# Optimization experiments

Hardware: AMD Instinct MI355X
Metric: run time of the kernel (lower is better)

The kernel has to match this reference:

```python
import jax, jax.numpy as jnp
import numpy as np

HIDDEN = 1024
EMB = 256
VOCAB = 500000
B = 4096
C = 128
EPS = 1e-12


def setup_inputs() -> dict:
    key = jax.random.key(0)
    ks = jax.random.split(key, 8)
    hidden_states = jax.random.normal(ks[0], (B, HIDDEN), dtype=jnp.float32)
    cand_idx = jax.random.randint(ks[1], (B, C), 0, VOCAB, dtype=jnp.int32)
    W_dense = jax.random.normal(ks[2], (EMB, HIDDEN), dtype=jnp.float32) * (1.0 / np.sqrt(HIDDEN))
    b_dense = jnp.zeros((EMB,), dtype=jnp.float32)
    ln_gamma = jnp.ones((EMB,), dtype=jnp.float32)
    ln_beta = jnp.zeros((EMB,), dtype=jnp.float32)
    decoder_table = jax.random.normal(ks[3], (VOCAB, EMB), dtype=jnp.float32) * 0.02
    entity_bias = jnp.zeros((VOCAB,), dtype=jnp.float32)
    return {
        "hidden_states": hidden_states,
        "W_dense": W_dense,
        "b_dense": b_dense,
        "ln_gamma": ln_gamma,
        "ln_beta": ln_beta,
        "decoder_table": decoder_table,
        "entity_bias": entity_bias,
        "cand_idx": cand_idx,
    }


def _transform(x, W_dense, b_dense, ln_gamma, ln_beta):
    # Linear hidden_size -> entity_emb_size, gelu, LayerNorm
    h = x @ W_dense.T + b_dense
    h = jax.nn.gelu(h, approximate=False)
    mu = jnp.mean(h, axis=-1, keepdims=True)
    var = jnp.mean(jnp.square(h - mu), axis=-1, keepdims=True)
    return (h - mu) * jax.lax.rsqrt(var + EPS) * ln_gamma + ln_beta


def reference(hidden_states, W_dense, b_dense, ln_gamma, ln_beta, decoder_table, entity_bias, cand_idx):
    h = _transform(hidden_states, W_dense, b_dense, ln_gamma, ln_beta)  # [B, EMB]
    cand_emb = decoder_table[cand_idx]          # [B, C, EMB] ragged gather (padded)
    bias = entity_bias[cand_idx]                # [B, C]
    scores = jnp.einsum('bce,be->bc', cand_emb, h) + bias  # [B, C]
    return scores
```

## Files before the change

### kernel.cpp

```cpp
#include <hip/hip_runtime.h>
#include <hip/hip_bf16.h>
#include <math.h>

#define HIDDEN 1024
#define EMB    256
#define BROWS  4096
#define CAND   128
#define LN_EPS 1e-12f

typedef __attribute__((ext_vector_type(8))) short bf16x8;
typedef __attribute__((ext_vector_type(4))) float f32x4;

__device__ __forceinline__ int swz(int row, int slot) { return slot ^ ((row >> 1) & 3); }

__device__ __forceinline__ unsigned short f2bf(float f) {
    __bf16 h = (__bf16)f;
    return __builtin_bit_cast(unsigned short, h);
}

__global__ __launch_bounds__(256) void k_transform(
    const float* __restrict__ A,
    const float* __restrict__ W,
    const float* __restrict__ bias,
    const float* __restrict__ gamma,
    const float* __restrict__ beta,
    float* __restrict__ G)
{
    __shared__ unsigned short As[64 * 32];
    __shared__ unsigned short Ws[256 * 32];
    __shared__ float part[64][8];

    const int tid  = threadIdx.x;
    const int lane = tid & 63;
    const int wv   = tid >> 6;
    const int m0   = blockIdx.x * 64;

    const int lcol = lane & 15;
    const int lk   = lane >> 4;

    const int arow = tid >> 2;
    const int apr  = tid & 3;

    f32x4 acc[4][4] = {};

    for (int kt = 0; kt < HIDDEN; kt += 32) {
        float4 a0 = *(const float4*)&A[(size_t)(m0 + arow) * HIDDEN + kt + apr * 8];
        float4 a1 = *(const float4*)&A[(size_t)(m0 + arow) * HIDDEN + kt + apr * 8 + 4];
        float4 w0[4], w1[4];
        #pragma unroll
        for (int i = 0; i < 4; ++i) {
            int id = tid + i * 256;
            int row = id >> 2, pr = id & 3;
            w0[i] = *(const float4*)&W[(size_t)row * HIDDEN + kt + pr * 8];
            w1[i] = *(const float4*)&W[(size_t)row * HIDDEN + kt + pr * 8 + 4];
        }
        __syncthreads();
        {
            bf16x8 v;
            v[0]=f2bf(a0.x); v[1]=f2bf(a0.y); v[2]=f2bf(a0.z); v[3]=f2bf(a0.w);
            v[4]=f2bf(a1.x); v[5]=f2bf(a1.y); v[6]=f2bf(a1.z); v[7]=f2bf(a1.w);
            *(bf16x8*)&As[arow * 32 + swz(arow, apr) * 8] = v;
        }
        #pragma unroll
        for (int i = 0; i < 4; ++i) {
            int id = tid + i * 256;
            int row = id >> 2, pr = id & 3;
            bf16x8 v;
            v[0]=f2bf(w0[i].x); v[1]=f2bf(w0[i].y); v[2]=f2bf(w0[i].z); v[3]=f2bf(w0[i].w);
            v[4]=f2bf(w1[i].x); v[5]=f2bf(w1[i].y); v[6]=f2bf(w1[i].z); v[7]=f2bf(w1[i].w);
            *(bf16x8*)&Ws[row * 32 + swz(row, pr) * 8] = v;
        }
        __syncthreads();
        bf16x8 af[4], bfr[4];
        #pragma unroll
        for (int m = 0; m < 4; ++m) {
            int r = m * 16 + lcol;
            af[m] = *(const bf16x8*)&As[r * 32 + swz(r, lk) * 8];
        }
        #pragma unroll
        for (int n = 0; n < 4; ++n) {
            int r = wv * 64 + n * 16 + lcol;
            bfr[n] = *(const bf16x8*)&Ws[r * 32 + swz(r, lk) * 8];
        }
        #pragma unroll
        for (int m = 0; m < 4; ++m)
            #pragma unroll
            for (int n = 0; n < 4; ++n)
                acc[m][n] = __builtin_amdgcn_mfma_f32_16x16x32_bf16(af[m], bfr[n], acc[m][n], 0, 0, 0);
    }

    float bcol[4], gcol[4], becol[4];
    #pragma unroll
    for (int n = 0; n < 4; ++n) {
        int col = wv * 64 + n * 16 + lcol;
        bcol[n]  = bias[col];
        gcol[n]  = gamma[col];
        becol[n] = beta[col];
    }

    float sv[4][4], qv[4][4];
    #pragma unroll
    for (int m = 0; m < 4; ++m) {
        #pragma unroll
        for (int r = 0; r < 4; ++r) { sv[m][r] = 0.0f; qv[m][r] = 0.0f; }
        #pragma unroll
        for (int n = 0; n < 4; ++n) {
            #pragma unroll
            for (int r = 0; r < 4; ++r) {
                float v = acc[m][n][r] + bcol[n];
                v = 0.5f * v * (1.0f + erff(v * 0.70710678118654752f));
                acc[m][n][r] = v;
                sv[m][r] += v;
                qv[m][r] += v * v;
            }
        }
        #pragma unroll
        for (int r = 0; r < 4; ++r) {
            #pragma unroll
            for (int msk = 8; msk >= 1; msk >>= 1) {
                sv[m][r] += __shfl_xor(sv[m][r], msk);
                qv[m][r] += __shfl_xor(qv[m][r], msk);
            }
        }
    }
    if (lcol == 0) {
        #pragma unroll
        for (int m = 0; m < 4; ++m)
            #pragma unroll
            for (int r = 0; r < 4; ++r) {
                int R = m * 16 + lk * 4 + r;
                part[R][wv * 2 + 0] = sv[m][r];
                part[R][wv * 2 + 1] = qv[m][r];
            }
    }
    __syncthreads();

    #pragma unroll
    for (int m = 0; m < 4; ++m) {
        #pragma unroll
        for (int r = 0; r < 4; ++r) {
            int R = m * 16 + lk * 4 + r;
            float4 p0 = *(const float4*)&part[R][0];
            float4 p1 = *(const float4*)&part[R][4];
            float s  = p0.x + p0.z + p1.x + p1.z;
            float q  = p0.y + p0.w + p1.y + p1.w;
            float mu = s * (1.0f / 256.0f);
            float var = q * (1.0f / 256.0f) - mu * mu;
            float rs = rsqrtf(var + LN_EPS);
            #pragma unroll
            for (int n = 0; n < 4; ++n) {
                int col = wv * 64 + n * 16 + lcol;
                G[(size_t)(m0 + R) * EMB + col] = (acc[m][n][r] - mu) * rs * gcol[n] + becol[n];
            }
        }
    }
}

__global__ __launch_bounds__(256) void k_scores(
    const float* __restrict__ H,
    const float* __restrict__ table,
    const float* __restrict__ ebias,
    const int*   __restrict__ cidx,
    float* __restrict__ out)
{
    __shared__ int sidx[CAND];
    const int b    = blockIdx.x;
    const int tid  = threadIdx.x;
    const int lane = tid & 63;
    const int wave = tid >> 6;

    if (tid < CAND) sidx[tid] = cidx[(size_t)b * CAND + tid];
    const float4 hv = *(const float4*)&H[(size_t)b * EMB + lane * 4];
    __syncthreads();

    #pragma unroll 2
    for (int i = 0; i < 32; ++i) {
        const int c   = wave * 32 + i;
        const int idx = sidx[c];
        const float4 tv = *(const float4*)&table[(size_t)idx * EMB + lane * 4];
        float s = tv.x * hv.x + tv.y * hv.y + tv.z * hv.z + tv.w * hv.w;
        #pragma unroll
        for (int m = 32; m >= 1; m >>= 1) s += __shfl_xor(s, m);
        if (lane == 0) out[(size_t)b * CAND + c] = s + ebias[idx];
    }
}

extern "C" void kernel_launch(void* const* d_in, const int* in_sizes, int n_in,
                              void* d_out, int out_size, void* d_ws, size_t ws_size,
                              hipStream_t stream) {
    const float* hidden = (const float*)d_in[0];
    const float* Wd     = (const float*)d_in[1];
    const float* bd     = (const float*)d_in[2];
    const float* gamma  = (const float*)d_in[3];
    const float* beta   = (const float*)d_in[4];
    const float* table  = (const float*)d_in[5];
    const float* ebias  = (const float*)d_in[6];
    const int*   cidx   = (const int*)d_in[7];
    float* out = (float*)d_out;

    float* G = (float*)d_ws;

    k_transform<<<dim3(BROWS / 64), 256, 0, stream>>>(hidden, Wd, bd, gamma, beta, G);
    k_scores<<<dim3(BROWS), 256, 0, stream>>>(G, table, ebias, cidx, out);
}
```

Before: 147.3 us.

## Shrink transform row tile and restructure gather to quarter-wave per candidate

The transform kernel's row tile drops from 64 to 16 rows per block, quadrupling the grid from 64 to 256 blocks so more compute units are busy, at the cost of re-reading W four times as often. The scores kernel now gives each 16-lane quarter-wave one candidate row and has each wave handle four candidates at once. All eight indices are loaded up front so the gathers can be issued together with more memory-level parallelism. This also drops the shared-memory index staging and the block barrier, and shortens the shuffle reduction.

```diff
diff --git a/kernel.cpp b/kernel.cpp
--- a/kernel.cpp
+++ b/kernel.cpp
@@ -26,26 +26,27 @@
     const float* __restrict__ beta,
     float* __restrict__ G)
 {
-    __shared__ unsigned short As[64 * 32];
+    __shared__ unsigned short As[16 * 32];
     __shared__ unsigned short Ws[256 * 32];
-    __shared__ float part[64][8];
+    __shared__ float part[16][8];
 
     const int tid  = threadIdx.x;
     const int lane = tid & 63;
     const int wv   = tid >> 6;
-    const int m0   = blockIdx.x * 64;
+    const int m0   = blockIdx.x * 16;
 
     const int lcol = lane & 15;
     const int lk   = lane >> 4;
 
-    const int arow = tid >> 2;
-    const int apr  = tid & 3;
-
-    f32x4 acc[4][4] = {};
+    f32x4 acc[4] = {};
 
     for (int kt = 0; kt < HIDDEN; kt += 32) {
-        float4 a0 = *(const float4*)&A[(size_t)(m0 + arow) * HIDDEN + kt + apr * 8];
-        float4 a1 = *(const float4*)&A[(size_t)(m0 + arow) * HIDDEN + kt + apr * 8 + 4];
+        float4 a0, a1;
+        const int arow = tid >> 2, apr = tid & 3;
+        if (tid < 64) {
+            a0 = *(const float4*)&A[(size_t)(m0 + arow) * HIDDEN + kt + apr * 8];
+            a1 = *(const float4*)&A[(size_t)(m0 + arow) * HIDDEN + kt + apr * 8 + 4];
+        }
         float4 w0[4], w1[4];
         #pragma unroll
         for (int i = 0; i < 4; ++i) {
@@ -55,7 +56,7 @@
             w1[i] = *(const float4*)&W[(size_t)row * HIDDEN + kt + pr * 8 + 4];
         }
         __syncthreads();
-        {
+        if (tid < 64) {
             bf16x8 v;
             v[0]=f2bf(a0.x); v[1]=f2bf(a0.y); v[2]=f2bf(a0.z); v[3]=f2bf(a0.w);
             v[4]=f2bf(a1.x); v[5]=f2bf(a1.y); v[6]=f2bf(a1.z); v[7]=f2bf(a1.w);
@@ -71,22 +72,16 @@
             *(bf16x8*)&Ws[row * 32 + swz(row, pr) * 8] = v;
         }
         __syncthreads();
-        bf16x8 af[4], bfr[4];
-        #pragma unroll
-        for (int m = 0; m < 4; ++m) {
-            int r = m * 16 + lcol;
-            af[m] = *(const bf16x8*)&As[r * 32 + swz(r, lk) * 8];
-        }
+        bf16x8 af = *(const bf16x8*)&As[lcol * 32 + swz(lcol, lk) * 8];
+        bf16x8 bfr[4];
         #pragma unroll
         for (int n = 0; n < 4; ++n) {
             int r = wv * 64 + n * 16 + lcol;
             bfr[n] = *(const bf16x8*)&Ws[r * 32 + swz(r, lk) * 8];
         }
         #pragma unroll
-        for (int m = 0; m < 4; ++m)
-            #pragma unroll
-            for (int n = 0; n < 4; ++n)
-                acc[m][n] = __builtin_amdgcn_mfma_f32_16x16x32_bf16(af[m], bfr[n], acc[m][n], 0, 0, 0);
+        for (int n = 0; n < 4; ++n)
+            acc[n] = __builtin_amdgcn_mfma_f32_16x16x32_bf16(af, bfr[n], acc[n], 0, 0, 0);
     }
 
     float bcol[4], gcol[4], becol[4];
@@ -98,60 +93,50 @@
         becol[n] = beta[col];
     }
 
-    float sv[4][4], qv[4][4];
-    #pragma unroll
-    for (int m = 0; m < 4; ++m) {
-        #pragma unroll
-        for (int r = 0; r < 4; ++r) { sv[m][r] = 0.0f; qv[m][r] = 0.0f; }
+    float sv[4] = {}, qv[4] = {};
+    #pragma unroll
+    for (int n = 0; n < 4; ++n) {
+        #pragma unroll
+        for (int r = 0; r < 4; ++r) {
+            float v = acc[n][r] + bcol[n];
+            v = 0.5f * v * (1.0f + erff(v * 0.70710678118654752f));
+            acc[n][r] = v;
+            sv[r] += v;
+            qv[r] += v * v;
+        }
+    }
+    #pragma unroll
+    for (int r = 0; r < 4; ++r) {
+        #pragma unroll
+        for (int msk = 8; msk >= 1; msk >>= 1) {
+            sv[r] += __shfl_xor(sv[r], msk);
+            qv[r] += __shfl_xor(qv[r], msk);
+        }
+    }
+    if (lcol == 0) {
+        #pragma unroll
+        for (int r = 0; r < 4; ++r) {
+            int R = lk * 4 + r;
+            part[R][wv * 2 + 0] = sv[r];
+            part[R][wv * 2 + 1] = qv[r];
+        }
+    }
+    __syncthreads();
+
+    #pragma unroll
+    for (int r = 0; r < 4; ++r) {
+        int R = lk * 4 + r;
+        float4 p0 = *(const float4*)&part[R][0];
+        float4 p1 = *(const float4*)&part[R][4];
+        float s  = p0.x + p0.z + p1.x + p1.z;
+        float q  = p0.y + p0.w + p1.y + p1.w;
+        float mu = s * (1.0f / 256.0f);
+        float var = q * (1.0f / 256.0f) - mu * mu;
+        float rs = rsqrtf(var + LN_EPS);
         #pragma unroll
         for (int n = 0; n < 4; ++n) {
-            #pragma unroll
-            for (int r = 0; r < 4; ++r) {
-                float v = acc[m][n][r] + bcol[n];
-                v = 0.5f * v * (1.0f + erff(v * 0.70710678118654752f));
-                acc[m][n][r] = v;
-                sv[m][r] += v;
-                qv[m][r] += v * v;
-            }
-        }
-        #pragma unroll
-        for (int r = 0; r < 4; ++r) {
-            #pragma unroll
-            for (int msk = 8; msk >= 1; msk >>= 1) {
-                sv[m][r] += __shfl_xor(sv[m][r], msk);
-                qv[m][r] += __shfl_xor(qv[m][r], msk);
-            }
-        }
-    }
-    if (lcol == 0) {
-        #pragma unroll
-        for (int m = 0; m < 4; ++m)
-            #pragma unroll
-            for (int r = 0; r < 4; ++r) {
-                int R = m * 16 + lk * 4 + r;
-                part[R][wv * 2 + 0] = sv[m][r];
-                part[R][wv * 2 + 1] = qv[m][r];
-            }
-    }
-    __syncthreads();
-
-    #pragma unroll
-    for (int m = 0; m < 4; ++m) {
-        #pragma unroll
-        for (int r = 0; r < 4; ++r) {
-            int R = m * 16 + lk * 4 + r;
-            float4 p0 = *(const float4*)&part[R][0];
-            float4 p1 = *(const float4*)&part[R][4];
-            float s  = p0.x + p0.z + p1.x + p1.z;
-            float q  = p0.y + p0.w + p1.y + p1.w;
-            float mu = s * (1.0f / 256.0f);
-            float var = q * (1.0f / 256.0f) - mu * mu;
-            float rs = rsqrtf(var + LN_EPS);
-            #pragma unroll
-            for (int n = 0; n < 4; ++n) {
-                int col = wv * 64 + n * 16 + lcol;
-                G[(size_t)(m0 + R) * EMB + col] = (acc[m][n][r] - mu) * rs * gcol[n] + becol[n];
-            }
+            int col = wv * 64 + n * 16 + lcol;
+            G[(size_t)(m0 + R) * EMB + col] = (acc[n][r] - mu) * rs * gcol[n] + becol[n];
         }
     }
 }
@@ -163,25 +148,39 @@
     const int*   __restrict__ cidx,
     float* __restrict__ out)
 {
-    __shared__ int sidx[CAND];
     const int b    = blockIdx.x;
     const int tid  = threadIdx.x;
     const int lane = tid & 63;
-    const int wave = tid >> 6;
-
-    if (tid < CAND) sidx[tid] = cidx[(size_t)b * CAND + tid];
-    const float4 hv = *(const float4*)&H[(size_t)b * EMB + lane * 4];
-    __syncthreads();
-
-    #pragma unroll 2
-    for (int i = 0; i < 32; ++i) {
-        const int c   = wave * 32 + i;
-        const int idx = sidx[c];
-        const float4 tv = *(const float4*)&table[(size_t)idx * EMB + lane * 4];
-        float s = tv.x * hv.x + tv.y * hv.y + tv.z * hv.z + tv.w * hv.w;
-        #pragma unroll
-        for (int m = 32; m >= 1; m >>= 1) s += __shfl_xor(s, m);
-        if (lane == 0) out[(size_t)b * CAND + c] = s + ebias[idx];
+    const int wv   = tid >> 6;
+    const int l    = lane & 15;
+    const int q    = lane >> 4;
+
+    const float4* Hrow = (const float4*)(H + (size_t)b * EMB);
+    float4 hv[4];
+    #pragma unroll
+    for (int p = 0; p < 4; ++p) hv[p] = Hrow[p * 16 + l];
+
+    const int cbase = wv * 32 + q;
+    int idxs[8];
+    #pragma unroll
+    for (int it = 0; it < 8; ++it)
+        idxs[it] = cidx[(size_t)b * CAND + cbase + it * 4];
+
+    #pragma unroll
+    for (int it = 0; it < 8; ++it) {
+        const float4* row = (const float4*)(table + (size_t)idxs[it] * EMB);
+        float4 t0 = row[ 0 + l];
+        float4 t1 = row[16 + l];
+        float4 t2 = row[32 + l];
+        float4 t3 = row[48 + l];
+        float  eb = ebias[idxs[it]];
+        float s = t0.x*hv[0].x + t0.y*hv[0].y + t0.z*hv[0].z + t0.w*hv[0].w
+                + t1.x*hv[1].x + t1.y*hv[1].y + t1.z*hv[1].z + t1.w*hv[1].w
+                + t2.x*hv[2].x + t2.y*hv[2].y + t2.z*hv[2].z + t2.w*hv[2].w
+                + t3.x*hv[3].x + t3.y*hv[3].y + t3.z*hv[3].z + t3.w*hv[3].w;
+        #pragma unroll
+        for (int m = 8; m >= 1; m >>= 1) s += __shfl_xor(s, m);
+        if (l == 0) out[(size_t)b * CAND + cbase + it * 4] = s + eb;
     }
 }
 
@@ -200,6 +199,6 @@
 
     float* G = (float*)d_ws;
 
-    k_transform<<<dim3(BROWS / 64), 256, 0, stream>>>(hidden, Wd, bd, gamma, beta, G);
+    k_transform<<<dim3(BROWS / 16), 256, 0, stream>>>(hidden, Wd, bd, gamma, beta, G);
     k_scores<<<dim3(BROWS), 256, 0, stream>>>(G, table, ebias, cidx, out);
 }
```

Result: faster. 135.6 us (-7.9%).
